# Optimization experiments

Measured on AMD Instinct MI355X. Metric: run time of the kernel, lower is better.

Reference implementation:

```python
import jax, jax.numpy as jnp
import numpy as np

N_HEADS = 32
N_KV_HEADS = 8
HEAD_DIM = 64
DIM = 2048
MAX_CTX = 2048
N_REP = N_HEADS // N_KV_HEADS


def setup_inputs() -> dict:
    key = jax.random.key(0)
    ks = jax.random.split(key, 8)
    B, S = 1, 2048
    x = jax.random.normal(ks[0], (B, S, DIM), dtype=jnp.float32)
    # RoPE frequencies (real cos/sin, [S, head_dim//2])
    inv_freq = 1.0 / (10000.0 ** (np.arange(0, HEAD_DIM, 2, dtype=np.float32) / HEAD_DIM))
    t = np.arange(S, dtype=np.float32)
    freqs = np.outer(t, inv_freq)  # [S, HEAD_DIM//2]
    freqs_cos = jnp.asarray(np.cos(freqs), dtype=jnp.float32)
    freqs_sin = jnp.asarray(np.sin(freqs), dtype=jnp.float32)
    input_pos = jnp.arange(S, dtype=jnp.int32)
    scale = 0.02
    wq = jax.random.normal(ks[1], (N_HEADS * HEAD_DIM, DIM), dtype=jnp.float32) * scale
    wk = jax.random.normal(ks[2], (N_KV_HEADS * HEAD_DIM, DIM), dtype=jnp.float32) * scale
    wv = jax.random.normal(ks[3], (N_KV_HEADS * HEAD_DIM, DIM), dtype=jnp.float32) * scale
    wo = jax.random.normal(ks[4], (DIM, N_HEADS * HEAD_DIM), dtype=jnp.float32) * scale
    k_cache = jnp.zeros((B, N_KV_HEADS, MAX_CTX, HEAD_DIM), dtype=jnp.float32)
    v_cache = jnp.zeros((B, N_KV_HEADS, MAX_CTX, HEAD_DIM), dtype=jnp.float32)
    return {"x": x, "freqs_cos": freqs_cos, "freqs_sin": freqs_sin,
            "input_pos": input_pos, "wq": wq, "wk": wk, "wv": wv, "wo": wo,
            "k_cache": k_cache, "v_cache": v_cache}


def _apply_rope(x, cos, sin):
    # x: [B, S, H, HEAD_DIM]; cos/sin: [S, HEAD_DIM//2]
    xr = x[..., 0::2]
    xi = x[..., 1::2]
    c = cos[None, :, None, :]
    s = sin[None, :, None, :]
    out_r = xr * c - xi * s
    out_i = xr * s + xi * c
    # interleave back: stack on new trailing axis then flatten pairs
    out = jnp.stack([out_r, out_i], axis=-1)
    return out.reshape(x.shape)


def reference(x, freqs_cos, freqs_sin, input_pos, wq, wk, wv, wo, k_cache, v_cache):
    B, S, _ = x.shape
    q = (x @ wq.T).reshape(B, S, N_HEADS, HEAD_DIM)
    k = (x @ wk.T).reshape(B, S, N_KV_HEADS, HEAD_DIM)
    v = (x @ wv.T).reshape(B, S, N_KV_HEADS, HEAD_DIM)
    q = _apply_rope(q, freqs_cos, freqs_sin)
    k = _apply_rope(k, freqs_cos, freqs_sin)
    q = q.transpose(0, 2, 1, 3)   # [B, H, S, D]
    k = k.transpose(0, 2, 1, 3)   # [B, KV, S, D]
    v = v.transpose(0, 2, 1, 3)
    # KV-cache scatter update at input_pos
    k_full = k_cache.at[:, :, input_pos].set(k)   # [B, KV, MAX_CTX, D]
    v_full = v_cache.at[:, :, input_pos].set(v)
    # causal mask rows gathered at input_pos: [S, MAX_CTX]
    causal = jnp.tril(jnp.ones((MAX_CTX, MAX_CTX), dtype=bool))
    attn_mask = causal[input_pos]
    # GQA repeat_interleave along head dim
    k_rep = jnp.repeat(k_full, N_REP, axis=1)    # [B, H, MAX_CTX, D]
    v_rep = jnp.repeat(v_full, N_REP, axis=1)
    scale = 1.0 / jnp.sqrt(jnp.asarray(HEAD_DIM, dtype=x.dtype))
    scores = jnp.einsum('bhsd,bhtd->bhst', q, k_rep) * scale  # [B, H, S, MAX_CTX]
    neg = jnp.asarray(jnp.finfo(scores.dtype).min, dtype=scores.dtype)
    scores = jnp.where(attn_mask[None, None, :, :], scores, neg)
    attn = jax.nn.softmax(scores, axis=-1)
    y = jnp.einsum('bhst,bhtd->bhsd', attn, v_rep)  # [B, H, S, D]
    y = y.transpose(0, 2, 1, 3).reshape(B, S, N_HEADS * HEAD_DIM)
    return y @ wo.T
```

## Files before the change

kernel.cpp:

```cpp
#include <hip/hip_runtime.h>


typedef __attribute__((ext_vector_type(8))) __bf16 bf16x8;
typedef __attribute__((ext_vector_type(4))) float f32x4;

#define S_LEN 2048
#define DIMN  2048
#define NH    32
#define NKV   8
#define HD    64
#define QKVF  3072

__device__ __forceinline__ ushort f2bf(float f) {
  union { float f; unsigned u; } v; v.f = f;
  unsigned r = v.u + 0x7fffu + ((v.u >> 16) & 1u);
  return (ushort)(r >> 16);
}
__device__ __forceinline__ unsigned pack_bf2_rz(float a, float b) {
  union { float f; unsigned u; } va, vb; va.f = a; vb.f = b;
  return (va.u >> 16) | (vb.u & 0xffff0000u);
}
__device__ __forceinline__ float bf2f(ushort u) {
  union { unsigned u; float f; } v; v.u = ((unsigned)u) << 16;
  return v.f;
}
__device__ __forceinline__ void gld_lds16(const void* g, void* l) {
  __builtin_amdgcn_global_load_lds(
      (const __attribute__((address_space(1))) unsigned int*)g,
      (__attribute__((address_space(3))) unsigned int*)l, 16, 0, 0);
}

__global__ __launch_bounds__(256) void convert_all(
    const float* __restrict__ x, const float* __restrict__ wq,
    const float* __restrict__ wk, const float* __restrict__ wv,
    const float* __restrict__ wo, ushort* __restrict__ xb,
    ushort* __restrict__ wqkvb, ushort* __restrict__ wob) {
  const size_t NX = 4u * 1024 * 1024;
  const size_t NK = 1024 * 1024;
  size_t idx = ((size_t)blockIdx.x * 256 + threadIdx.x) * 4;
  const float* src; ushort* dst;
  if (idx < NX)                { src = x  + idx;                  dst = xb + idx; }
  else if (idx < 2 * NX)       { src = wq + (idx - NX);           dst = wqkvb + (idx - NX); }
  else if (idx < 2 * NX + NK)  { src = wk + (idx - 2 * NX);       dst = wqkvb + NX + (idx - 2 * NX); }
  else if (idx < 2 * NX + 2*NK){ src = wv + (idx - 2 * NX - NK);  dst = wqkvb + NX + NK + (idx - 2 * NX - NK); }
  else                         { src = wo + (idx - 2 * NX - 2*NK);dst = wob + (idx - 2 * NX - 2 * NK); }
  float4 v = *(const float4*)src;
  ushort4 o; o.x = f2bf(v.x); o.y = f2bf(v.y); o.z = f2bf(v.z); o.w = f2bf(v.w);
  *(ushort4*)dst = o;
}

template <int OUT_BF16, int BM, int BN>
__global__ __launch_bounds__(256) void gemm_bt(
    const ushort* __restrict__ A, const ushort* __restrict__ B,
    void* __restrict__ Cv, int M, int N, int K) {
  constexpr int IB = BM / 32;
  constexpr int JB = BN / 32;
  constexpr int NGA = BM / 8;
  constexpr int GPW = (BM + BN) / 32;
  __shared__ __align__(16) ushort As[2][BM * 64];
  __shared__ __align__(16) ushort Bs[2][BN * 64];
  const int n0 = blockIdx.x * BN, m0 = blockIdx.y * BM;
  const int t = threadIdx.x;
  const int lane = t & 63, wave = t >> 6;
  const int wm = (wave >> 1) * (BM / 2), wn = (wave & 1) * (BN / 2);
  const int col = lane & 15, quad = lane >> 4;
  const int sw = col & 7;
  const int lrow = lane >> 3;
  const int scol = ((lane & 7) ^ lrow) * 8;
  f32x4 acc[IB][JB] = {};

  auto stage = [&](int b, int kk) {
#pragma unroll
    for (int c = 0; c < GPW; ++c) {
      int g = wave * GPW + c;
      if (g < NGA)
        gld_lds16(&A[(size_t)(m0 + g * 8 + lrow) * K + kk + scol], &As[b][g * 8 * 64]);
      else
        gld_lds16(&B[(size_t)(n0 + (g - NGA) * 8 + lrow) * K + kk + scol],
                  &Bs[b][(g - NGA) * 8 * 64]);
    }
  };

  stage(0, 0);
  __syncthreads();
  for (int kk = 0; kk < K; kk += 64) {
    const int b = (kk >> 6) & 1;
    if (kk + 64 < K) stage(b ^ 1, kk + 64);
#pragma unroll
    for (int c = 0; c < 2; ++c) {
      const int chs = ((c * 4 + quad) ^ sw) * 8;
      bf16x8 af[IB], bfr[JB];
#pragma unroll
      for (int i = 0; i < IB; ++i)
        af[i] = *(const bf16x8*)&As[b][(wm + i * 16 + col) * 64 + chs];
#pragma unroll
      for (int j = 0; j < JB; ++j)
        bfr[j] = *(const bf16x8*)&Bs[b][(wn + j * 16 + col) * 64 + chs];
#pragma unroll
      for (int i = 0; i < IB; ++i)
#pragma unroll
        for (int j = 0; j < JB; ++j)
          acc[i][j] = __builtin_amdgcn_mfma_f32_16x16x32_bf16(af[i], bfr[j], acc[i][j], 0, 0, 0);
    }
    __syncthreads();
  }
#pragma unroll
  for (int i = 0; i < IB; ++i)
#pragma unroll
    for (int r = 0; r < 4; ++r) {
      int m = m0 + wm + i * 16 + quad * 4 + r;
      if (OUT_BF16) {
        ushort* C = (ushort*)Cv;
#pragma unroll
        for (int j = 0; j < JB; ++j)
          C[(size_t)m * N + n0 + wn + j * 16 + col] = f2bf(acc[i][j][r]);
      } else {
        float* C = (float*)Cv;
#pragma unroll
        for (int j = 0; j < JB; ++j)
          C[(size_t)m * N + n0 + wn + j * 16 + col] = acc[i][j][r];
      }
    }
}

__global__ __launch_bounds__(256) void rope_layout(
    const ushort* __restrict__ qkv, const float* __restrict__ fc,
    const float* __restrict__ fs, ushort* __restrict__ qb,
    ushort* __restrict__ kb, ushort* __restrict__ vt) {
  __shared__ ushort T[64][72];
  const int hh = blockIdx.x;
  const int s0 = blockIdx.y * 256;
  const int t = threadIdx.x;
  if (hh < 32) {
    ushort* dst = qb + (size_t)hh * S_LEN * 64;
    const float qs = 0.18033688011112042f;
    const int sr = t >> 4, dc = (t & 15) * 4, i0 = (t & 15) * 2;
#pragma unroll 4
    for (int pass = 0; pass < 16; ++pass) {
      int s = s0 + pass * 16 + sr;
      ushort4 vv = *(const ushort4*)&qkv[(size_t)s * QKVF + hh * 64 + dc];
      float2 cc = *(const float2*)&fc[s * 32 + i0];
      float2 ss = *(const float2*)&fs[s * 32 + i0];
      float xr0 = bf2f(vv.x), xi0 = bf2f(vv.y), xr1 = bf2f(vv.z), xi1 = bf2f(vv.w);
      ushort4 ov;
      ov.x = f2bf((xr0 * cc.x - xi0 * ss.x) * qs); ov.y = f2bf((xr0 * ss.x + xi0 * cc.x) * qs);
      ov.z = f2bf((xr1 * cc.y - xi1 * ss.y) * qs); ov.w = f2bf((xr1 * ss.y + xi1 * cc.y) * qs);
      *(ushort4*)&dst[(size_t)s * 64 + dc] = ov;
    }
  } else if (hh < 40) {
    const int kh2 = hh - 32;
    const int sr8 = t >> 3;
    const int ch = t & 7;
#pragma unroll 2
    for (int pass = 0; pass < 8; ++pass) {
      int s = s0 + pass * 32 + sr8;
      ushort in[8], out[8];
      *(int4*)&in[0] = *(const int4*)&qkv[(size_t)s * QKVF + 2048 + kh2 * 64 + ch * 8];
      float4 cc = *(const float4*)&fc[s * 32 + ch * 4];
      float4 ss4 = *(const float4*)&fs[s * 32 + ch * 4];
      const float* cp = &cc.x; const float* sp = &ss4.x;
#pragma unroll
      for (int i = 0; i < 4; ++i) {
        float xr = bf2f(in[2 * i]), xi = bf2f(in[2 * i + 1]);
        out[2 * i]     = f2bf(xr * cp[i] - xi * sp[i]);
        out[2 * i + 1] = f2bf(xr * sp[i] + xi * cp[i]);
      }
      int r = s & 63, tile = s >> 6;
      size_t pos = ((size_t)(kh2 * 32 + tile)) * 4096 + (r * 8 + (ch ^ (r & 7))) * 8;
      *(int4*)&kb[pos] = *(const int4*)&out[0];
    }
  } else {
    const int vh = hh - 40;
    for (int sub = 0; sub < 4; ++sub) {
      int sb = s0 + sub * 64;
      int sr = t >> 2, dc = (t & 3) * 16;
      ushort tmp[16];
      *(int4*)&tmp[0] = *(const int4*)&qkv[(size_t)(sb + sr) * QKVF + 2560 + vh * 64 + dc];
      *(int4*)&tmp[8] = *(const int4*)&qkv[(size_t)(sb + sr) * QKVF + 2560 + vh * 64 + dc + 8];
      __syncthreads();
      const int pcol = ((sr & 15) << 2) | (sr >> 4);
#pragma unroll
      for (int k = 0; k < 16; ++k) T[dc + k][pcol] = tmp[k];
      __syncthreads();
      int d = t >> 2;
      int ch0 = (t & 3) * 2, ch1 = ch0 + 1;
      int tile = sb >> 6;
      size_t base = ((size_t)(vh * 32 + tile)) * 4096;
      *(int4*)&vt[base + (d * 8 + (ch0 ^ (d & 7))) * 8] = *(const int4*)&T[d][ch0 * 8];
      *(int4*)&vt[base + (d * 8 + (ch1 ^ (d & 7))) * 8] = *(const int4*)&T[d][ch1 * 8];
    }
  }
}

__global__ __launch_bounds__(256, 2) void attn(
    const ushort* __restrict__ qbg, const ushort* __restrict__ kbg,
    const ushort* __restrict__ vtg, ushort* __restrict__ yb) {
  __shared__ __align__(16) ushort Ks[2][4096];
  __shared__ __align__(16) ushort Vs[2][4096];
  __shared__ __align__(16) ushort Ps[4][16][64];
  const int kvh = blockIdx.x;
  const int s = blockIdx.y;
  const int wave = threadIdx.x >> 6;
  const int lane = threadIdx.x & 63;
  const int col = lane & 15, quad = lane >> 4;
  const int h = kvh * 4 + wave;
  const ushort* qh = qbg + (size_t)h * S_LEN * HD;
  const ushort* kbase = kbg + (size_t)kvh * 32 * 4096;
  const ushort* vbase = vtg + (size_t)kvh * 32 * 4096;
  const int rsw = col & 7;

  auto stage = [&](int tile, int buf) {
#pragma unroll
    for (int g = 0; g < 2; ++g) {
      int gg = wave + g * 4;
      gld_lds16(kbase + (size_t)tile * 4096 + gg * 512 + lane * 8, &Ks[buf][gg * 512]);
      gld_lds16(vbase + (size_t)tile * 4096 + gg * 512 + lane * 8, &Vs[buf][gg * 512]);
    }
  };

  const int nt = (s >> 2) + 1;
  const int q0 = s * 16;
  bf16x8 qf[2];
  qf[0] = *(const bf16x8*)&qh[(size_t)(q0 + col) * HD + quad * 8];
  qf[1] = *(const bf16x8*)&qh[(size_t)(q0 + col) * HD + 32 + quad * 8];
  float l[4] = {};
  f32x4 o[4] = {};
  stage(0, 0);
  __syncthreads();
  for (int t = 0; t < nt; ++t) {
    const int buf = t & 1;
    if (t + 1 < nt) stage(t + 1, buf ^ 1);
    f32x4 sc[4] = {};
#pragma unroll
    for (int c = 0; c < 2; ++c) {
      const int chs = (c * 4 + quad) ^ rsw;
#pragma unroll
      for (int j = 0; j < 4; ++j) {
        bf16x8 kf = *(const bf16x8*)&Ks[buf][((j * 16 + col) * 8 + chs) * 8];
        sc[j] = __builtin_amdgcn_mfma_f32_16x16x32_bf16(qf[c], kf, sc[j], 0, 0, 0);
      }
    }
    const bool masked = (t == nt - 1);
#pragma unroll
    for (int r = 0; r < 4; ++r) {
      const int rowq = q0 + quad * 4 + r;
      float pr[4];
#pragma unroll
      for (int j = 0; j < 4; ++j) {
        float e = __builtin_amdgcn_exp2f(sc[j][r]);
        if (masked) e = (t * 64 + j * 16 + col > rowq) ? 0.f : e;
        pr[j] = e;
      }
      l[r] += (pr[0] + pr[1]) + (pr[2] + pr[3]);
      uint2 pk;
      pk.x = pack_bf2_rz(pr[0], pr[1]);
      pk.y = pack_bf2_rz(pr[2], pr[3]);
      const int prow = quad * 4 + r;
      *(uint2*)&Ps[wave][prow][(((col >> 1) ^ (prow & 7)) << 3) + ((col & 1) << 2)] = pk;
    }
#pragma unroll
    for (int c = 0; c < 2; ++c) {
      const int chs = (c * 4 + quad) ^ rsw;
      bf16x8 pf = *(const bf16x8*)&Ps[wave][col][((c * 4 + quad) ^ (col & 7)) * 8];
#pragma unroll
      for (int db = 0; db < 4; ++db) {
        bf16x8 vf = *(const bf16x8*)&Vs[buf][((db * 16 + col) * 8 + chs) * 8];
        o[db] = __builtin_amdgcn_mfma_f32_16x16x32_bf16(pf, vf, o[db], 0, 0, 0);
      }
    }
    __syncthreads();
  }
#pragma unroll
  for (int r = 0; r < 4; ++r) {
    float ls = l[r];
    ls += __shfl_xor(ls, 1);
    ls += __shfl_xor(ls, 2);
    ls += __shfl_xor(ls, 4);
    ls += __shfl_xor(ls, 8);
    float inv = 1.0f / ls;
    int rowq = q0 + quad * 4 + r;
#pragma unroll
    for (int db = 0; db < 4; ++db)
      yb[(size_t)rowq * (NH * HD) + h * HD + db * 16 + col] = f2bf(o[db][r] * inv);
  }
}

extern "C" void kernel_launch(void* const* d_in, const int* in_sizes, int n_in,
                              void* d_out, int out_size, void* d_ws, size_t ws_size,
                              hipStream_t stream) {
  (void)in_sizes; (void)n_in; (void)out_size; (void)ws_size;
  const float* x  = (const float*)d_in[0];
  const float* fc = (const float*)d_in[1];
  const float* fs = (const float*)d_in[2];
  const float* wq = (const float*)d_in[4];
  const float* wk = (const float*)d_in[5];
  const float* wv = (const float*)d_in[6];
  const float* wo = (const float*)d_in[7];
  ushort* w = (ushort*)d_ws;
  const size_t M1 = 1024 * 1024;
  ushort* xb    = w;
  ushort* wqkvb = w + 4 * M1;
  ushort* wob   = w + 10 * M1;
  ushort* qkvb  = w + 14 * M1;
  ushort* qb    = w + 20 * M1;
  ushort* kb    = w + 24 * M1;
  ushort* vt    = w + 25 * M1;
  ushort* yb    = w + 26 * M1;

  convert_all<<<14336, 256, 0, stream>>>(x, wq, wk, wv, wo, xb, wqkvb, wob);
  gemm_bt<1, 128, 96><<<dim3(QKVF / 96, S_LEN / 128), 256, 0, stream>>>(xb, wqkvb, qkvb, S_LEN, QKVF, DIMN);
  rope_layout<<<dim3(48, 8), 256, 0, stream>>>(qkvb, fc, fs, qb, kb, vt);
  attn<<<dim3(NKV, 128), 256, 0, stream>>>(qb, kb, vt, yb);
  gemm_bt<0, 64, 128><<<dim3(DIMN / 128, S_LEN / 64), 256, 0, stream>>>(yb, wob, d_out, S_LEN, DIMN, NH * HD);
}
```

Baseline: 216.7 us.

## Pair causal query tiles per block and read K/V fragments directly from global

Each attention block now handles two 16-row query tiles, y and 127-y, so causal work is balanced across blocks and the grid is halved. The shared K/V tiles become the operands of both tiles' MFMAs wherever the two overlap. The LDS staging through global_load_lds and the per-tile barriers are removed; K and Vt are written by rope_layout in an MFMA-fragment-native order so each lane reads its fragment straight from global memory or cache. This trades LDS traffic and sync for more global or L2 loads per wave, each wave loading the K/V it needs without sharing across waves, and higher register pressure from two sets of accumulators.

```diff
diff --git a/kernel.cpp b/kernel.cpp
--- a/kernel.cpp
+++ b/kernel.cpp
@@ -10,6 +10,9 @@
 #define NKV   8
 #define HD    64
 #define QKVF  3072
+
+struct DoPair { static constexpr bool value = true; };
+struct OnlyB  { static constexpr bool value = false; };
 
 __device__ __forceinline__ ushort f2bf(float f) {
   union { float f; unsigned u; } v; v.f = f;
@@ -166,7 +169,8 @@
         out[2 * i + 1] = f2bf(xr * sp[i] + xi * cp[i]);
       }
       int r = s & 63, tile = s >> 6;
-      size_t pos = ((size_t)(kh2 * 32 + tile)) * 4096 + (r * 8 + (ch ^ (r & 7))) * 8;
+      size_t pos = ((size_t)(kh2 * 32 + tile)) * 4096 +
+                   ((size_t)(((ch >> 2) * 4 + (r >> 4)) * 64 + (ch & 3) * 16 + (r & 15))) * 8;
       *(int4*)&kb[pos] = *(const int4*)&out[0];
     }
   } else {
@@ -186,8 +190,10 @@
       int ch0 = (t & 3) * 2, ch1 = ch0 + 1;
       int tile = sb >> 6;
       size_t base = ((size_t)(vh * 32 + tile)) * 4096;
-      *(int4*)&vt[base + (d * 8 + (ch0 ^ (d & 7))) * 8] = *(const int4*)&T[d][ch0 * 8];
-      *(int4*)&vt[base + (d * 8 + (ch1 ^ (d & 7))) * 8] = *(const int4*)&T[d][ch1 * 8];
+      size_t p0 = base + ((size_t)(((ch0 >> 2) * 4 + (d >> 4)) * 64 + (ch0 & 3) * 16 + (d & 15))) * 8;
+      size_t p1 = base + ((size_t)(((ch1 >> 2) * 4 + (d >> 4)) * 64 + (ch1 & 3) * 16 + (d & 15))) * 8;
+      *(int4*)&vt[p0] = *(const int4*)&T[d][ch0 * 8];
+      *(int4*)&vt[p1] = *(const int4*)&T[d][ch1 * 8];
     }
   }
 }
@@ -195,11 +201,12 @@
 __global__ __launch_bounds__(256, 2) void attn(
     const ushort* __restrict__ qbg, const ushort* __restrict__ kbg,
     const ushort* __restrict__ vtg, ushort* __restrict__ yb) {
-  __shared__ __align__(16) ushort Ks[2][4096];
-  __shared__ __align__(16) ushort Vs[2][4096];
-  __shared__ __align__(16) ushort Ps[4][16][64];
+  __shared__ __align__(16) ushort Ps[4][2][16][64];
   const int kvh = blockIdx.x;
-  const int s = blockIdx.y;
+  const int y = blockIdx.y;
+  const int sA = y, sB = 127 - y;
+  const int ntA = (sA >> 2) + 1;
+  const int ntB = (sB >> 2) + 1;
   const int wave = threadIdx.x >> 6;
   const int lane = threadIdx.x & 63;
   const int col = lane & 15, quad = lane >> 4;
@@ -207,82 +214,104 @@
   const ushort* qh = qbg + (size_t)h * S_LEN * HD;
   const ushort* kbase = kbg + (size_t)kvh * 32 * 4096;
   const ushort* vbase = vtg + (size_t)kvh * 32 * 4096;
-  const int rsw = col & 7;
-
-  auto stage = [&](int tile, int buf) {
-#pragma unroll
-    for (int g = 0; g < 2; ++g) {
-      int gg = wave + g * 4;
-      gld_lds16(kbase + (size_t)tile * 4096 + gg * 512 + lane * 8, &Ks[buf][gg * 512]);
-      gld_lds16(vbase + (size_t)tile * 4096 + gg * 512 + lane * 8, &Vs[buf][gg * 512]);
+
+  const int q0A = sA * 16, q0B = sB * 16;
+  bf16x8 qfA[2], qfB[2];
+  qfA[0] = *(const bf16x8*)&qh[(size_t)(q0A + col) * HD + quad * 8];
+  qfA[1] = *(const bf16x8*)&qh[(size_t)(q0A + col) * HD + 32 + quad * 8];
+  qfB[0] = *(const bf16x8*)&qh[(size_t)(q0B + col) * HD + quad * 8];
+  qfB[1] = *(const bf16x8*)&qh[(size_t)(q0B + col) * HD + 32 + quad * 8];
+  float lA[4] = {}, lB[4] = {};
+  f32x4 oA[4] = {}, oB[4] = {};
+
+  auto tile_body = [&](int t, bool maskA, bool maskB, auto tag) {
+    constexpr bool DOA = decltype(tag)::value;
+    const ushort* kt  = kbase + (size_t)t * 4096;
+    const ushort* vtt = vbase + (size_t)t * 4096;
+    f32x4 scA[4] = {}, scB[4] = {};
+#pragma unroll
+    for (int c = 0; c < 2; ++c) {
+#pragma unroll
+      for (int j = 0; j < 4; ++j) {
+        bf16x8 kf = *(const bf16x8*)&kt[((c * 4 + j) * 64 + lane) * 8];
+        scB[j] = __builtin_amdgcn_mfma_f32_16x16x32_bf16(qfB[c], kf, scB[j], 0, 0, 0);
+        if constexpr (DOA)
+          scA[j] = __builtin_amdgcn_mfma_f32_16x16x32_bf16(qfA[c], kf, scA[j], 0, 0, 0);
+      }
+    }
+#pragma unroll
+    for (int r = 0; r < 4; ++r) {
+      const int prow = quad * 4 + r;
+      const int psw = (((col >> 1) ^ (prow & 7)) << 3) + ((col & 1) << 2);
+      {
+        const int rowq = q0B + prow;
+        float pr[4];
+#pragma unroll
+        for (int j = 0; j < 4; ++j) {
+          float e = __builtin_amdgcn_exp2f(scB[j][r]);
+          if (maskB) e = (t * 64 + j * 16 + col > rowq) ? 0.f : e;
+          pr[j] = e;
+        }
+        lB[r] += (pr[0] + pr[1]) + (pr[2] + pr[3]);
+        uint2 pk;
+        pk.x = pack_bf2_rz(pr[0], pr[1]);
+        pk.y = pack_bf2_rz(pr[2], pr[3]);
+        *(uint2*)&Ps[wave][1][prow][psw] = pk;
+      }
+      if constexpr (DOA) {
+        const int rowq = q0A + prow;
+        float pr[4];
+#pragma unroll
+        for (int j = 0; j < 4; ++j) {
+          float e = __builtin_amdgcn_exp2f(scA[j][r]);
+          if (maskA) e = (t * 64 + j * 16 + col > rowq) ? 0.f : e;
+          pr[j] = e;
+        }
+        lA[r] += (pr[0] + pr[1]) + (pr[2] + pr[3]);
+        uint2 pk;
+        pk.x = pack_bf2_rz(pr[0], pr[1]);
+        pk.y = pack_bf2_rz(pr[2], pr[3]);
+        *(uint2*)&Ps[wave][0][prow][psw] = pk;
+      }
+    }
+#pragma unroll
+    for (int c = 0; c < 2; ++c) {
+      const int psr = ((c * 4 + quad) ^ (col & 7)) * 8;
+      bf16x8 pfB = *(const bf16x8*)&Ps[wave][1][col][psr];
+      bf16x8 pfA;
+      if constexpr (DOA) pfA = *(const bf16x8*)&Ps[wave][0][col][psr];
+#pragma unroll
+      for (int db = 0; db < 4; ++db) {
+        bf16x8 vf = *(const bf16x8*)&vtt[((c * 4 + db) * 64 + lane) * 8];
+        oB[db] = __builtin_amdgcn_mfma_f32_16x16x32_bf16(pfB, vf, oB[db], 0, 0, 0);
+        if constexpr (DOA)
+          oA[db] = __builtin_amdgcn_mfma_f32_16x16x32_bf16(pfA, vf, oA[db], 0, 0, 0);
+      }
     }
   };
 
-  const int nt = (s >> 2) + 1;
-  const int q0 = s * 16;
-  bf16x8 qf[2];
-  qf[0] = *(const bf16x8*)&qh[(size_t)(q0 + col) * HD + quad * 8];
-  qf[1] = *(const bf16x8*)&qh[(size_t)(q0 + col) * HD + 32 + quad * 8];
-  float l[4] = {};
-  f32x4 o[4] = {};
-  stage(0, 0);
-  __syncthreads();
-  for (int t = 0; t < nt; ++t) {
-    const int buf = t & 1;
-    if (t + 1 < nt) stage(t + 1, buf ^ 1);
-    f32x4 sc[4] = {};
-#pragma unroll
-    for (int c = 0; c < 2; ++c) {
-      const int chs = (c * 4 + quad) ^ rsw;
-#pragma unroll
-      for (int j = 0; j < 4; ++j) {
-        bf16x8 kf = *(const bf16x8*)&Ks[buf][((j * 16 + col) * 8 + chs) * 8];
-        sc[j] = __builtin_amdgcn_mfma_f32_16x16x32_bf16(qf[c], kf, sc[j], 0, 0, 0);
-      }
-    }
-    const bool masked = (t == nt - 1);
+  int t = 0;
+  for (; t < ntA; ++t) tile_body(t, t == ntA - 1, false, DoPair{});
+  for (; t < ntB - 1; ++t) tile_body(t, false, false, OnlyB{});
+  tile_body(ntB - 1, false, true, OnlyB{});
+
+  auto write_out = [&](const f32x4 (&o)[4], const float (&l)[4], int q0) {
 #pragma unroll
     for (int r = 0; r < 4; ++r) {
-      const int rowq = q0 + quad * 4 + r;
-      float pr[4];
-#pragma unroll
-      for (int j = 0; j < 4; ++j) {
-        float e = __builtin_amdgcn_exp2f(sc[j][r]);
-        if (masked) e = (t * 64 + j * 16 + col > rowq) ? 0.f : e;
-        pr[j] = e;
-      }
-      l[r] += (pr[0] + pr[1]) + (pr[2] + pr[3]);
-      uint2 pk;
-      pk.x = pack_bf2_rz(pr[0], pr[1]);
-      pk.y = pack_bf2_rz(pr[2], pr[3]);
-      const int prow = quad * 4 + r;
-      *(uint2*)&Ps[wave][prow][(((col >> 1) ^ (prow & 7)) << 3) + ((col & 1) << 2)] = pk;
-    }
-#pragma unroll
-    for (int c = 0; c < 2; ++c) {
-      const int chs = (c * 4 + quad) ^ rsw;
-      bf16x8 pf = *(const bf16x8*)&Ps[wave][col][((c * 4 + quad) ^ (col & 7)) * 8];
-#pragma unroll
-      for (int db = 0; db < 4; ++db) {
-        bf16x8 vf = *(const bf16x8*)&Vs[buf][((db * 16 + col) * 8 + chs) * 8];
-        o[db] = __builtin_amdgcn_mfma_f32_16x16x32_bf16(pf, vf, o[db], 0, 0, 0);
-      }
-    }
-    __syncthreads();
-  }
-#pragma unroll
-  for (int r = 0; r < 4; ++r) {
-    float ls = l[r];
-    ls += __shfl_xor(ls, 1);
-    ls += __shfl_xor(ls, 2);
-    ls += __shfl_xor(ls, 4);
-    ls += __shfl_xor(ls, 8);
-    float inv = 1.0f / ls;
-    int rowq = q0 + quad * 4 + r;
-#pragma unroll
-    for (int db = 0; db < 4; ++db)
-      yb[(size_t)rowq * (NH * HD) + h * HD + db * 16 + col] = f2bf(o[db][r] * inv);
-  }
+      float ls = l[r];
+      ls += __shfl_xor(ls, 1);
+      ls += __shfl_xor(ls, 2);
+      ls += __shfl_xor(ls, 4);
+      ls += __shfl_xor(ls, 8);
+      float inv = 1.0f / ls;
+      int rowq = q0 + quad * 4 + r;
+#pragma unroll
+      for (int db = 0; db < 4; ++db)
+        yb[(size_t)rowq * (NH * HD) + h * HD + db * 16 + col] = f2bf(o[db][r] * inv);
+    }
+  };
+  write_out(oA, lA, q0A);
+  write_out(oB, lB, q0B);
 }
 
 extern "C" void kernel_launch(void* const* d_in, const int* in_sizes, int n_in,
@@ -310,6 +339,6 @@
   convert_all<<<14336, 256, 0, stream>>>(x, wq, wk, wv, wo, xb, wqkvb, wob);
   gemm_bt<1, 128, 96><<<dim3(QKVF / 96, S_LEN / 128), 256, 0, stream>>>(xb, wqkvb, qkvb, S_LEN, QKVF, DIMN);
   rope_layout<<<dim3(48, 8), 256, 0, stream>>>(qkvb, fc, fs, qb, kb, vt);
-  attn<<<dim3(NKV, 128), 256, 0, stream>>>(qb, kb, vt, yb);
+  attn<<<dim3(NKV, 64), 256, 0, stream>>>(qb, kb, vt, yb);
   gemm_bt<0, 64, 128><<<dim3(DIMN / 128, S_LEN / 64), 256, 0, stream>>>(yb, wob, d_out, S_LEN, DIMN, NH * HD);
 }
```

Result: faster. 211.8 us (-2.3%).

## Restructure attention: balanced causal query blocks, split-K waves, register K/V fragments

Applied to the files above, without the earlier changes.

The attention kernel now gives each block four 16-row query tiles paired for causal load balance (y, 63-y, 64+y, 127-y). It splits the key tiles between two wave halves that are merged through shared memory at the end. K and V are rewritten by the rope/layout kernel into an MFMA-fragment-ready layout, so each lane loads its fragments straight from global memory into registers instead of staging through double-buffered LDS. This drops the per-tile __syncthreads and LDS staging and reuses each loaded K/V tile across four query tiles. In exchange it uses more registers (16 accumulators per lane) and adds redundant global loads across waves, which could lower occupancy.

```diff
diff --git a/kernel.cpp b/kernel.cpp
--- a/kernel.cpp
+++ b/kernel.cpp
@@ -166,7 +166,8 @@
         out[2 * i + 1] = f2bf(xr * sp[i] + xi * cp[i]);
       }
       int r = s & 63, tile = s >> 6;
-      size_t pos = ((size_t)(kh2 * 32 + tile)) * 4096 + (r * 8 + (ch ^ (r & 7))) * 8;
+      size_t pos = ((size_t)(kh2 * 32 + tile)) * 4096 +
+                   ((size_t)(((ch >> 2) * 4 + (r >> 4)) * 64 + (ch & 3) * 16 + (r & 15))) * 8;
       *(int4*)&kb[pos] = *(const int4*)&out[0];
     }
   } else {
@@ -186,102 +187,131 @@
       int ch0 = (t & 3) * 2, ch1 = ch0 + 1;
       int tile = sb >> 6;
       size_t base = ((size_t)(vh * 32 + tile)) * 4096;
-      *(int4*)&vt[base + (d * 8 + (ch0 ^ (d & 7))) * 8] = *(const int4*)&T[d][ch0 * 8];
-      *(int4*)&vt[base + (d * 8 + (ch1 ^ (d & 7))) * 8] = *(const int4*)&T[d][ch1 * 8];
-    }
-  }
-}
-
-__global__ __launch_bounds__(256, 2) void attn(
+      size_t p0 = base + ((size_t)(((ch0 >> 2) * 4 + (d >> 4)) * 64 + (ch0 & 3) * 16 + (d & 15))) * 8;
+      size_t p1 = base + ((size_t)(((ch1 >> 2) * 4 + (d >> 4)) * 64 + (ch1 & 3) * 16 + (d & 15))) * 8;
+      *(int4*)&vt[p0] = *(const int4*)&T[d][ch0 * 8];
+      *(int4*)&vt[p1] = *(const int4*)&T[d][ch1 * 8];
+    }
+  }
+}
+
+__global__ __launch_bounds__(512, 2) void attn(
     const ushort* __restrict__ qbg, const ushort* __restrict__ kbg,
     const ushort* __restrict__ vtg, ushort* __restrict__ yb) {
-  __shared__ __align__(16) ushort Ks[2][4096];
-  __shared__ __align__(16) ushort Vs[2][4096];
-  __shared__ __align__(16) ushort Ps[4][16][64];
+  __shared__ __align__(16) ushort Ps[8][2][16][64];
+  __shared__ __align__(16) float Mrg[4][64][21];
   const int kvh = blockIdx.x;
-  const int s = blockIdx.y;
+  const int y = blockIdx.y;
   const int wave = threadIdx.x >> 6;
   const int lane = threadIdx.x & 63;
+  const int hw = wave & 3, khalf = wave >> 2;
   const int col = lane & 15, quad = lane >> 4;
-  const int h = kvh * 4 + wave;
+  const int h = kvh * 4 + hw;
   const ushort* qh = qbg + (size_t)h * S_LEN * HD;
   const ushort* kbase = kbg + (size_t)kvh * 32 * 4096;
   const ushort* vbase = vtg + (size_t)kvh * 32 * 4096;
-  const int rsw = col & 7;
-
-  auto stage = [&](int tile, int buf) {
-#pragma unroll
-    for (int g = 0; g < 2; ++g) {
-      int gg = wave + g * 4;
-      gld_lds16(kbase + (size_t)tile * 4096 + gg * 512 + lane * 8, &Ks[buf][gg * 512]);
-      gld_lds16(vbase + (size_t)tile * 4096 + gg * 512 + lane * 8, &Vs[buf][gg * 512]);
-    }
-  };
-
-  const int nt = (s >> 2) + 1;
-  const int q0 = s * 16;
-  bf16x8 qf[2];
-  qf[0] = *(const bf16x8*)&qh[(size_t)(q0 + col) * HD + quad * 8];
-  qf[1] = *(const bf16x8*)&qh[(size_t)(q0 + col) * HD + 32 + quad * 8];
-  float l[4] = {};
-  f32x4 o[4] = {};
-  stage(0, 0);
-  __syncthreads();
-  for (int t = 0; t < nt; ++t) {
-    const int buf = t & 1;
-    if (t + 1 < nt) stage(t + 1, buf ^ 1);
-    f32x4 sc[4] = {};
-#pragma unroll
-    for (int c = 0; c < 2; ++c) {
-      const int chs = (c * 4 + quad) ^ rsw;
-#pragma unroll
-      for (int j = 0; j < 4; ++j) {
-        bf16x8 kf = *(const bf16x8*)&Ks[buf][((j * 16 + col) * 8 + chs) * 8];
-        sc[j] = __builtin_amdgcn_mfma_f32_16x16x32_bf16(qf[c], kf, sc[j], 0, 0, 0);
+
+  int s[4], nt[4], q0[4];
+  s[0] = y; s[1] = 63 - y; s[2] = 64 + y; s[3] = 127 - y;
+#pragma unroll
+  for (int i = 0; i < 4; ++i) { nt[i] = (s[i] >> 2) + 1; q0[i] = s[i] * 16; }
+
+  bf16x8 qf[4][2];
+#pragma unroll
+  for (int i = 0; i < 4; ++i) {
+    qf[i][0] = *(const bf16x8*)&qh[(size_t)(q0[i] + col) * HD + quad * 8];
+    qf[i][1] = *(const bf16x8*)&qh[(size_t)(q0[i] + col) * HD + 32 + quad * 8];
+  }
+  float l[4][4] = {};
+  f32x4 o[4][4] = {};
+
+  const int ntmax = nt[3];
+  for (int t = khalf; t < ntmax; t += 2) {
+    const ushort* kt  = kbase + (size_t)t * 4096;
+    const ushort* vtt = vbase + (size_t)t * 4096;
+    bf16x8 kf[8], vf[8];
+#pragma unroll
+    for (int p = 0; p < 8; ++p) kf[p] = *(const bf16x8*)&kt[(p * 64 + lane) * 8];
+#pragma unroll
+    for (int p = 0; p < 8; ++p) vf[p] = *(const bf16x8*)&vtt[(p * 64 + lane) * 8];
+#pragma unroll
+    for (int i = 0; i < 4; ++i) {
+      if (t < nt[i]) {
+        f32x4 sc[4] = {};
+#pragma unroll
+        for (int c = 0; c < 2; ++c)
+#pragma unroll
+          for (int j = 0; j < 4; ++j)
+            sc[j] = __builtin_amdgcn_mfma_f32_16x16x32_bf16(qf[i][c], kf[c * 4 + j], sc[j], 0, 0, 0);
+        const bool masked = (t == nt[i] - 1);
+#pragma unroll
+        for (int r = 0; r < 4; ++r) {
+          const int prow = quad * 4 + r;
+          const int rowq = q0[i] + prow;
+          float pr[4];
+#pragma unroll
+          for (int j = 0; j < 4; ++j) {
+            float e = __builtin_amdgcn_exp2f(sc[j][r]);
+            if (masked) e = (t * 64 + j * 16 + col > rowq) ? 0.f : e;
+            pr[j] = e;
+          }
+          l[i][r] += (pr[0] + pr[1]) + (pr[2] + pr[3]);
+          uint2 pk;
+          pk.x = pack_bf2_rz(pr[0], pr[1]);
+          pk.y = pack_bf2_rz(pr[2], pr[3]);
+          const int psw = (((col >> 1) ^ (prow & 7)) << 3) + ((col & 1) << 2);
+          *(uint2*)&Ps[wave][i & 1][prow][psw] = pk;
+        }
+#pragma unroll
+        for (int c = 0; c < 2; ++c) {
+          bf16x8 pf = *(const bf16x8*)&Ps[wave][i & 1][col][((c * 4 + quad) ^ (col & 7)) * 8];
+#pragma unroll
+          for (int db = 0; db < 4; ++db)
+            o[i][db] = __builtin_amdgcn_mfma_f32_16x16x32_bf16(pf, vf[c * 4 + db], o[i][db], 0, 0, 0);
+        }
       }
     }
-    const bool masked = (t == nt - 1);
-#pragma unroll
-    for (int r = 0; r < 4; ++r) {
-      const int rowq = q0 + quad * 4 + r;
-      float pr[4];
-#pragma unroll
-      for (int j = 0; j < 4; ++j) {
-        float e = __builtin_amdgcn_exp2f(sc[j][r]);
-        if (masked) e = (t * 64 + j * 16 + col > rowq) ? 0.f : e;
-        pr[j] = e;
+  }
+
+#pragma unroll
+  for (int i = 0; i < 4; ++i) {
+    if (khalf == 1) {
+#pragma unroll
+      for (int db = 0; db < 4; ++db)
+#pragma unroll
+        for (int r = 0; r < 4; ++r) Mrg[hw][lane][db * 4 + r] = o[i][db][r];
+#pragma unroll
+      for (int r = 0; r < 4; ++r) Mrg[hw][lane][16 + r] = l[i][r];
+    }
+    __syncthreads();
+    if (khalf == 0) {
+#pragma unroll
+      for (int db = 0; db < 4; ++db)
+#pragma unroll
+        for (int r = 0; r < 4; ++r) o[i][db][r] += Mrg[hw][lane][db * 4 + r];
+#pragma unroll
+      for (int r = 0; r < 4; ++r) l[i][r] += Mrg[hw][lane][16 + r];
+    }
+    __syncthreads();
+  }
+
+  if (khalf == 0) {
+#pragma unroll
+    for (int i = 0; i < 4; ++i) {
+#pragma unroll
+      for (int r = 0; r < 4; ++r) {
+        float ls = l[i][r];
+        ls += __shfl_xor(ls, 1);
+        ls += __shfl_xor(ls, 2);
+        ls += __shfl_xor(ls, 4);
+        ls += __shfl_xor(ls, 8);
+        float inv = 1.0f / ls;
+        int rowq = q0[i] + quad * 4 + r;
+#pragma unroll
+        for (int db = 0; db < 4; ++db)
+          yb[(size_t)rowq * (NH * HD) + h * HD + db * 16 + col] = f2bf(o[i][db][r] * inv);
       }
-      l[r] += (pr[0] + pr[1]) + (pr[2] + pr[3]);
-      uint2 pk;
-      pk.x = pack_bf2_rz(pr[0], pr[1]);
-      pk.y = pack_bf2_rz(pr[2], pr[3]);
-      const int prow = quad * 4 + r;
-      *(uint2*)&Ps[wave][prow][(((col >> 1) ^ (prow & 7)) << 3) + ((col & 1) << 2)] = pk;
-    }
-#pragma unroll
-    for (int c = 0; c < 2; ++c) {
-      const int chs = (c * 4 + quad) ^ rsw;
-      bf16x8 pf = *(const bf16x8*)&Ps[wave][col][((c * 4 + quad) ^ (col & 7)) * 8];
-#pragma unroll
-      for (int db = 0; db < 4; ++db) {
-        bf16x8 vf = *(const bf16x8*)&Vs[buf][((db * 16 + col) * 8 + chs) * 8];
-        o[db] = __builtin_amdgcn_mfma_f32_16x16x32_bf16(pf, vf, o[db], 0, 0, 0);
-      }
-    }
-    __syncthreads();
-  }
-#pragma unroll
-  for (int r = 0; r < 4; ++r) {
-    float ls = l[r];
-    ls += __shfl_xor(ls, 1);
-    ls += __shfl_xor(ls, 2);
-    ls += __shfl_xor(ls, 4);
-    ls += __shfl_xor(ls, 8);
-    float inv = 1.0f / ls;
-    int rowq = q0 + quad * 4 + r;
-#pragma unroll
-    for (int db = 0; db < 4; ++db)
-      yb[(size_t)rowq * (NH * HD) + h * HD + db * 16 + col] = f2bf(o[db][r] * inv);
+    }
   }
 }
 
@@ -310,6 +340,6 @@
   convert_all<<<14336, 256, 0, stream>>>(x, wq, wk, wv, wo, xb, wqkvb, wob);
   gemm_bt<1, 128, 96><<<dim3(QKVF / 96, S_LEN / 128), 256, 0, stream>>>(xb, wqkvb, qkvb, S_LEN, QKVF, DIMN);
   rope_layout<<<dim3(48, 8), 256, 0, stream>>>(qkvb, fc, fs, qb, kb, vt);
-  attn<<<dim3(NKV, 128), 256, 0, stream>>>(qb, kb, vt, yb);
+  attn<<<dim3(NKV, 32), 512, 0, stream>>>(qb, kb, vt, yb);
   gemm_bt<0, 64, 128><<<dim3(DIMN / 128, S_LEN / 64), 256, 0, stream>>>(yb, wob, d_out, S_LEN, DIMN, NH * HD);
 }
```

Result: no change. 214.1 us (-1.2%).
